# Performance work log

Hardware: AMD Instinct MI355X
Metric: run time of the kernel (lower is better)

The kernel has to match this reference:

```python
import jax, jax.numpy as jnp
import numpy as np

H = 1024      # hidden_size
V = 50257     # output_size (vocab)
L = 100       # max_length


def setup_inputs() -> dict:
    key = jax.random.key(0)
    ks = jax.random.split(key, 14)
    s = 0.02
    return {
        "token": jax.random.randint(ks[0], (1,), 0, V),
        "hidden": jax.random.normal(ks[1], (1, 1, H), jnp.float32),
        "encoder_outputs": jax.random.normal(ks[2], (L, H), jnp.float32),
        "embedding": jax.random.normal(ks[3], (V, H), jnp.float32) * s,
        "attn_w": jax.random.normal(ks[4], (L, 2 * H), jnp.float32) * s,
        "attn_b": jnp.zeros((L,), jnp.float32),
        "comb_w": jax.random.normal(ks[5], (H, 2 * H), jnp.float32) * s,
        "comb_b": jnp.zeros((H,), jnp.float32),
        "w_ih": jax.random.normal(ks[6], (3 * H, H), jnp.float32) * s,
        "w_hh": jax.random.normal(ks[7], (3 * H, H), jnp.float32) * s,
        "b_ih": jnp.zeros((3 * H,), jnp.float32),
        "b_hh": jnp.zeros((3 * H,), jnp.float32),
        "out_w": jax.random.normal(ks[8], (V, H), jnp.float32) * s,
        "out_b": jnp.zeros((V,), jnp.float32),
    }


def reference(token, hidden, encoder_outputs, embedding, attn_w, attn_b,
              comb_w, comb_b, w_ih, w_hh, b_ih, b_hh, out_w, out_b):
    # embedding lookup; dropout is identity in eval mode
    emb = embedding[token]                                   # [1, H]
    h0 = hidden[0]                                           # [1, H]
    # attention over encoder positions
    attn_in = jnp.concatenate([emb, h0], axis=1)             # [1, 2H]
    attn_weights = jax.nn.softmax(attn_in @ attn_w.T + attn_b, axis=1)  # [1, L]
    attn_applied = attn_weights @ encoder_outputs            # [1, H]
    # combine + relu
    x = jnp.concatenate([emb, attn_applied], axis=1) @ comb_w.T + comb_b  # [1, H]
    x = jax.nn.relu(x)
    # single GRU cell step (PyTorch gate order: r, z, n)
    gi = x @ w_ih.T + b_ih                                   # [1, 3H]
    gh = h0 @ w_hh.T + b_hh                                  # [1, 3H]
    ir, iz, in_ = jnp.split(gi, 3, axis=1)
    hr, hz, hn = jnp.split(gh, 3, axis=1)
    r = jax.nn.sigmoid(ir + hr)
    z = jax.nn.sigmoid(iz + hz)
    n = jnp.tanh(in_ + r * hn)
    h_new = (1.0 - z) * n + z * h0                           # [1, H]
    # output projection + log_softmax
    output = jax.nn.log_softmax(h_new @ out_w.T + out_b, axis=1)  # [1, V]
    return output, h_new[None], attn_weights
```

## Files before the change

### kernel.cpp

```cpp
#include <hip/hip_runtime.h>
#include <hip/hip_bf16.h>

#define H 1024
#define V 50257
#define L 100
#define NDB 2048


__device__ __forceinline__ float wave_sum(float v) {
    #pragma unroll
    for (int off = 32; off > 0; off >>= 1) v += __shfl_down(v, off, 64);
    return v;
}

__device__ __forceinline__ float dot1024(const float4* w, const float4* x, int lane) {
    float acc = 0.f;
    #pragma unroll
    for (int j = 0; j < 4; j++) {
        float4 a = w[lane + 64 * j];
        float4 b = x[lane + 64 * j];
        acc += a.x * b.x + a.y * b.y + a.z * b.z + a.w * b.w;
    }
    return acc;
}


__global__ void k1_head(const int* token, const float* hidden, const float* embedding,
                        const float* attn_w, const float* attn_b,
                        const float* w_hh, const float* b_hh,
                        float* ws_log, float* ws_gh) {
    int lane = threadIdx.x & 63, wv = threadIdx.x >> 6;
    const float4* e4 = (const float4*)(embedding + (size_t)token[0] * H);
    const float4* h4 = (const float4*)hidden;
    if (blockIdx.x < 25) {
        int r = blockIdx.x * 4 + wv;
        const float4* wr = (const float4*)(attn_w + (size_t)r * (2 * H));
        float acc = dot1024(wr, e4, lane) + dot1024(wr + 256, h4, lane);
        acc = wave_sum(acc);
        if (lane == 0) ws_log[r] = acc + attn_b[r];
    } else {
        int r = (blockIdx.x - 25) * 4 + wv;
        const float4* wr = (const float4*)(w_hh + (size_t)r * H);
        float acc = wave_sum(dot1024(wr, h4, lane));
        if (lane == 0) ws_gh[r] = acc + b_hh[r];
    }
}


__global__ void k2_mid(const int* token, const float* ws_log, const float* enc,
                       const float* embedding, const float* comb_w, const float* comb_b,
                       float* ws_x, float* out_attnw) {
    __shared__ float red[8];
    __shared__ float aw[128];
    __shared__ float4 app4[256];
    int t = threadIdx.x, lane = t & 63, wv = t >> 6;

    float x = (t < L) ? ws_log[t] : -1e30f;
    float mv = x;
    #pragma unroll
    for (int off = 32; off > 0; off >>= 1) mv = fmaxf(mv, __shfl_down(mv, off, 64));
    if (lane == 0) red[wv] = mv;
    __syncthreads();
    float m = fmaxf(fmaxf(red[0], red[1]), fmaxf(red[2], red[3]));
    float e = (t < L) ? expf(x - m) : 0.f;
    float sv = wave_sum(e);
    if (lane == 0) red[4 + wv] = sv;
    __syncthreads();
    float s = red[4] + red[5] + red[6] + red[7];
    float a = e / s;
    if (t < 128) aw[t] = a;
    if (blockIdx.x == 0 && t < L) out_attnw[t] = a;
    __syncthreads();

    {
        const float4* enc4 = (const float4*)enc;
        float4 acc4 = make_float4(0.f, 0.f, 0.f, 0.f);
        #pragma unroll 4
        for (int l = 0; l < L; l++) {
            float w = aw[l];
            float4 ev = enc4[l * 256 + t];
            acc4.x += w * ev.x; acc4.y += w * ev.y;
            acc4.z += w * ev.z; acc4.w += w * ev.w;
        }
        app4[t] = acc4;
    }
    __syncthreads();

    const float4* e4 = (const float4*)(embedding + (size_t)token[0] * H);
    #pragma unroll
    for (int k = 0; k < 2; k++) {
        int r = blockIdx.x * 8 + wv * 2 + k;
        const float4* wr = (const float4*)(comb_w + (size_t)r * (2 * H));
        float acc = dot1024(wr, e4, lane) + dot1024(wr + 256, app4, lane);
        acc = wave_sum(acc);
        if (lane == 0) ws_x[r] = fmaxf(acc + comb_b[r], 0.0f);
    }
}


__global__ void k3_gru(const float* ws_x, const float* hidden, const float* ws_gh,
                       const float* w_ih, const float* b_ih, const float* b_hh,
                       float* out_h, float* ws_hn) {
    int lane = threadIdx.x & 63, wv = threadIdx.x >> 6;
    int h = blockIdx.x * 4 + wv;
    const float4* x4 = (const float4*)ws_x;
    float a0 = dot1024((const float4*)(w_ih + (size_t)h * H), x4, lane);
    float a1 = dot1024((const float4*)(w_ih + (size_t)(H + h) * H), x4, lane);
    float a2 = dot1024((const float4*)(w_ih + (size_t)(2 * H + h) * H), x4, lane);
    a0 = wave_sum(a0); a1 = wave_sum(a1); a2 = wave_sum(a2);
    if (lane == 0) {
        float ir = a0 + b_ih[h], iz = a1 + b_ih[H + h], in_ = a2 + b_ih[2 * H + h];
        float hr = ws_gh[h] , hz = ws_gh[H + h],  hn = ws_gh[2 * H + h];
        float r = 1.f / (1.f + expf(-(ir + hr)));
        float z = 1.f / (1.f + expf(-(iz + hz)));
        float n = tanhf(in_ + r * hn);
        float h0 = hidden[h];
        float v = (1.f - z) * n + z * h0;
        out_h[h] = v;
        ws_hn[h] = v;
    }
}


__global__ void kD_outproj(const float* hn, const float* out_w, const float* out_b,
                           float* out_logits, float* ws_pm, float* ws_ps) {
    __shared__ float sm[4], ss[4];
    int lane = threadIdx.x & 63;
    int wv   = threadIdx.x >> 6;
    const float4* h4 = (const float4*)hn;
    float4 h0 = h4[lane], h1 = h4[lane + 64], h2 = h4[lane + 128], h3 = h4[lane + 192];
    float m = -1e30f, s = 0.f;
    int wid = blockIdx.x * 4 + wv;
    for (int r0 = wid * 2; r0 < V; r0 += NDB * 8) {
        float acc[2] = {0.f, 0.f};
        #pragma unroll
        for (int i = 0; i < 2; i++) {
            int r = r0 + i;
            if (r < V) {
                const float4* wr = (const float4*)(out_w + (size_t)r * H);
                float4 a = wr[lane], b = wr[lane + 64], c = wr[lane + 128], d = wr[lane + 192];
                acc[i] = a.x * h0.x + a.y * h0.y + a.z * h0.z + a.w * h0.w
                       + b.x * h1.x + b.y * h1.y + b.z * h1.z + b.w * h1.w
                       + c.x * h2.x + c.y * h2.y + c.z * h2.z + c.w * h2.w
                       + d.x * h3.x + d.y * h3.y + d.z * h3.z + d.w * h3.w;
            }
        }
        #pragma unroll
        for (int off = 32; off > 0; off >>= 1) {
            acc[0] += __shfl_down(acc[0], off, 64);
            acc[1] += __shfl_down(acc[1], off, 64);
        }
        if (lane == 0) {
            #pragma unroll
            for (int i = 0; i < 2; i++) {
                int r = r0 + i;
                if (r < V) {
                    float lg = acc[i] + out_b[r];
                    out_logits[r] = lg;
                    float nm = fmaxf(m, lg);
                    s = s * expf(m - nm) + expf(lg - nm);
                    m = nm;
                }
            }
        }
    }
    if (lane == 0) { sm[wv] = m; ss[wv] = s; }
    __syncthreads();
    if (threadIdx.x == 0) {
        m = sm[0]; s = ss[0];
        #pragma unroll
        for (int i = 1; i < 4; i++) {
            float nm = fmaxf(m, sm[i]);
            s = s * expf(m - nm) + ss[i] * expf(sm[i] - nm);
            m = nm;
        }
        ws_pm[blockIdx.x] = m;
        ws_ps[blockIdx.x] = s;
    }
}


__global__ void kE_finalize(const float* ws_pm, const float* ws_ps, float* out) {
    __shared__ float sm[4], ss[4], fm, fs;
    int t = threadIdx.x;
    float m = -1e30f, s = 0.f;
    for (int i = t; i < NDB; i += 256) {
        float pm = ws_pm[i], ps = ws_ps[i];
        float nm = fmaxf(m, pm);
        s = s * expf(m - nm) + ps * expf(pm - nm);
        m = nm;
    }
    #pragma unroll
    for (int off = 32; off > 0; off >>= 1) {
        float om = __shfl_down(m, off, 64);
        float os = __shfl_down(s, off, 64);
        float nm = fmaxf(m, om);
        s = s * expf(m - nm) + os * expf(om - nm);
        m = nm;
    }
    int lane = t & 63, wv = t >> 6;
    if (lane == 0) { sm[wv] = m; ss[wv] = s; }
    __syncthreads();
    if (t == 0) {
        m = sm[0]; s = ss[0];
        #pragma unroll
        for (int i = 1; i < 4; i++) {
            float nm = fmaxf(m, sm[i]);
            s = s * expf(m - nm) + ss[i] * expf(sm[i] - nm);
            m = nm;
        }
        fm = m; fs = logf(s);
    }
    __syncthreads();
    float M = fm, LS = fs;
    for (int v = blockIdx.x * 256 + t; v < V; v += gridDim.x * 256)
        out[v] = out[v] - M - LS;
}


extern "C" void kernel_launch(void* const* d_in, const int* in_sizes, int n_in,
                              void* d_out, int out_size, void* d_ws, size_t ws_size,
                              hipStream_t stream) {
    const int*   token     = (const int*)d_in[0];
    const float* hidden    = (const float*)d_in[1];
    const float* enc       = (const float*)d_in[2];
    const float* embedding = (const float*)d_in[3];
    const float* attn_w    = (const float*)d_in[4];
    const float* attn_b    = (const float*)d_in[5];
    const float* comb_w    = (const float*)d_in[6];
    const float* comb_b    = (const float*)d_in[7];
    const float* w_ih      = (const float*)d_in[8];
    const float* w_hh      = (const float*)d_in[9];
    const float* b_ih      = (const float*)d_in[10];
    const float* b_hh      = (const float*)d_in[11];
    const float* out_w     = (const float*)d_in[12];
    const float* out_b     = (const float*)d_in[13];

    float* out = (float*)d_out;
    float* ws  = (float*)d_ws;
    float* ws_log = ws;
    float* ws_gh  = ws + 128;
    float* ws_x   = ws + 3200;
    float* ws_pm  = ws + 4224;
    float* ws_ps  = ws + 6272;
    float* ws_hn  = ws + 8320;

    k1_head<<<dim3(793), dim3(256), 0, stream>>>(token, hidden, embedding,
                                                 attn_w, attn_b, w_hh, b_hh,
                                                 ws_log, ws_gh);
    k2_mid<<<dim3(128), dim3(256), 0, stream>>>(token, ws_log, enc, embedding,
                                                comb_w, comb_b, ws_x, out + V + H);
    k3_gru<<<dim3(256), dim3(256), 0, stream>>>(ws_x, hidden, ws_gh, w_ih, b_ih, b_hh,
                                                out + V, ws_hn);
    kD_outproj<<<dim3(NDB), dim3(256), 0, stream>>>(ws_hn, out_w, out_b, out, ws_pm, ws_ps);
    kE_finalize<<<dim3(128), dim3(256), 0, stream>>>(ws_pm, ws_ps, out);
}
```

Measured before the change: 63.75 us.

## Split softmax-attention apply from comb projection to stop redundant per-block work

The old middle kernel had each of its 128 blocks redo the softmax and the full 100x1024 attention-weighted sum over encoder outputs before computing 8 comb rows. Now a 16-block kernel computes the softmax and the weighted sum once, with the sequence dimension split across waves, and writes it to workspace. A separate 256-block kernel computes the comb projection at one row per wave. This removes 128x redundant reads of the encoder outputs at the cost of an extra kernel launch and a global round trip.

Measured after the change: 56.96 us. 1.12x faster.

```diff
diff --git a/kernel.cpp b/kernel.cpp
--- a/kernel.cpp
+++ b/kernel.cpp
@@ -30,9 +30,9 @@
                         const float* w_hh, const float* b_hh,
                         float* ws_log, float* ws_gh) {
     int lane = threadIdx.x & 63, wv = threadIdx.x >> 6;
-    const float4* e4 = (const float4*)(embedding + (size_t)token[0] * H);
     const float4* h4 = (const float4*)hidden;
     if (blockIdx.x < 25) {
+        const float4* e4 = (const float4*)(embedding + (size_t)token[0] * H);
         int r = blockIdx.x * 4 + wv;
         const float4* wr = (const float4*)(attn_w + (size_t)r * (2 * H));
         float acc = dot1024(wr, e4, lane) + dot1024(wr + 256, h4, lane);
@@ -47,12 +47,11 @@
 }
 
 
-__global__ void k2_mid(const int* token, const float* ws_log, const float* enc,
-                       const float* embedding, const float* comb_w, const float* comb_b,
-                       float* ws_x, float* out_attnw) {
+__global__ void kS_softmax_apply(const float* ws_log, const float* enc,
+                                 float* ws_app, float* out_attnw) {
     __shared__ float red[8];
-    __shared__ float aw[128];
-    __shared__ float4 app4[256];
+    __shared__ float aw_s[128];
+    __shared__ float part[4][64];
     int t = threadIdx.x, lane = t & 63, wv = t >> 6;
 
     float x = (t < L) ? ws_log[t] : -1e30f;
@@ -67,34 +66,35 @@
     if (lane == 0) red[4 + wv] = sv;
     __syncthreads();
     float s = red[4] + red[5] + red[6] + red[7];
-    float a = e / s;
-    if (t < 128) aw[t] = a;
-    if (blockIdx.x == 0 && t < L) out_attnw[t] = a;
-    __syncthreads();
-
-    {
-        const float4* enc4 = (const float4*)enc;
-        float4 acc4 = make_float4(0.f, 0.f, 0.f, 0.f);
-        #pragma unroll 4
-        for (int l = 0; l < L; l++) {
-            float w = aw[l];
-            float4 ev = enc4[l * 256 + t];
-            acc4.x += w * ev.x; acc4.y += w * ev.y;
-            acc4.z += w * ev.z; acc4.w += w * ev.w;
-        }
-        app4[t] = acc4;
-    }
-    __syncthreads();
-
+    float aw = e / s;
+    if (t < 128) aw_s[t] = aw;
+    if (blockIdx.x == 0 && t < L) out_attnw[t] = aw;
+    __syncthreads();
+
+    int h = blockIdx.x * 64 + lane;
+    float acc = 0.f;
+    #pragma unroll
+    for (int i = 0; i < 25; i++) {
+        int l = wv * 25 + i;
+        acc += aw_s[l] * enc[l * H + h];
+    }
+    part[wv][lane] = acc;
+    __syncthreads();
+    if (wv == 0)
+        ws_app[h] = part[0][lane] + part[1][lane] + part[2][lane] + part[3][lane];
+}
+
+
+__global__ void kComb(const int* token, const float* embedding, const float* ws_app,
+                      const float* comb_w, const float* comb_b, float* ws_x) {
+    int lane = threadIdx.x & 63, wv = threadIdx.x >> 6;
+    int r = blockIdx.x * 4 + wv;
     const float4* e4 = (const float4*)(embedding + (size_t)token[0] * H);
-    #pragma unroll
-    for (int k = 0; k < 2; k++) {
-        int r = blockIdx.x * 8 + wv * 2 + k;
-        const float4* wr = (const float4*)(comb_w + (size_t)r * (2 * H));
-        float acc = dot1024(wr, e4, lane) + dot1024(wr + 256, app4, lane);
-        acc = wave_sum(acc);
-        if (lane == 0) ws_x[r] = fmaxf(acc + comb_b[r], 0.0f);
-    }
+    const float4* a4 = (const float4*)ws_app;
+    const float4* wr = (const float4*)(comb_w + (size_t)r * (2 * H));
+    float acc = dot1024(wr, e4, lane) + dot1024(wr + 256, a4, lane);
+    acc = wave_sum(acc);
+    if (lane == 0) ws_x[r] = fmaxf(acc + comb_b[r], 0.0f);
 }
 
 
@@ -240,16 +240,18 @@
     float* ws  = (float*)d_ws;
     float* ws_log = ws;
     float* ws_gh  = ws + 128;
-    float* ws_x   = ws + 3200;
-    float* ws_pm  = ws + 4224;
-    float* ws_ps  = ws + 6272;
-    float* ws_hn  = ws + 8320;
+    float* ws_app = ws + 3200;
+    float* ws_x   = ws + 4224;
+    float* ws_pm  = ws + 5248;
+    float* ws_ps  = ws + 7296;
+    float* ws_hn  = ws + 9344;
 
     k1_head<<<dim3(793), dim3(256), 0, stream>>>(token, hidden, embedding,
                                                  attn_w, attn_b, w_hh, b_hh,
                                                  ws_log, ws_gh);
-    k2_mid<<<dim3(128), dim3(256), 0, stream>>>(token, ws_log, enc, embedding,
-                                                comb_w, comb_b, ws_x, out + V + H);
+    kS_softmax_apply<<<dim3(16), dim3(256), 0, stream>>>(ws_log, enc, ws_app, out + V + H);
+    kComb<<<dim3(256), dim3(256), 0, stream>>>(token, embedding, ws_app,
+                                               comb_w, comb_b, ws_x);
     k3_gru<<<dim3(256), dim3(256), 0, stream>>>(ws_x, hidden, ws_gh, w_ih, b_ih, b_hh,
                                                 out + V, ws_hn);
     kD_outproj<<<dim3(NDB), dim3(256), 0, stream>>>(ws_hn, out_w, out_b, out, ws_pm, ws_ps);
```
